# Kernel optimization log

Measured on AMD Instinct MI355X. Metric: run time of the kernel, lower is better.

The kernel has to match this reference:

```python
import jax, jax.numpy as jnp
import numpy as np

GRID_SIZE = 5
IMG_H, IMG_W = 256, 192
N_CTRL = GRID_SIZE * GRID_SIZE
RBF_SCALE = 10.0
OFFSET_SCALE = 0.3


def _source_pts():
    # control points on a [-0.9, 0.9] lattice, (N, 2) as (x, y)
    s = jnp.linspace(-0.9, 0.9, GRID_SIZE)
    gy, gx = jnp.meshgrid(s, s, indexing='ij')
    return jnp.stack([gx.ravel(), gy.ravel()], axis=-1)


def _tps_grid(theta):
    B = theta.shape[0]
    src = _source_pts()                                   # (N, 2)
    offsets = theta.reshape(B, N_CTRL, 2) * OFFSET_SCALE  # dx,dy per control pt
    gy = jnp.linspace(-1.0, 1.0, IMG_H)
    gx = jnp.linspace(-1.0, 1.0, IMG_W)
    my, mx = jnp.meshgrid(gy, gx, indexing='ij')          # (H, W)
    # RBF basis per control point: (N, H, W)
    dist = (mx[None] - src[:, 0, None, None]) ** 2 + (my[None] - src[:, 1, None, None]) ** 2
    w = jnp.exp(-dist * RBF_SCALE)
    # accumulate all control-point displacements in one contraction (fused loop)
    ox = jnp.einsum('bn,nhw->bhw', offsets[..., 0], w)
    oy = jnp.einsum('bn,nhw->bhw', offsets[..., 1], w)
    grid = jnp.stack([mx[None] + ox, my[None] + oy], axis=-1)  # (B, H, W, 2)
    return jnp.clip(grid, -1.0, 1.0)


def _grid_sample_border(img, grid):
    # bilinear grid_sample, align_corners=True, padding_mode='border'
    B, C, H, W = img.shape
    x = (grid[..., 0] + 1.0) * 0.5 * (W - 1)
    y = (grid[..., 1] + 1.0) * 0.5 * (H - 1)
    x0f = jnp.floor(x)
    y0f = jnp.floor(y)
    wx = x - x0f
    wy = y - y0f
    x0 = jnp.clip(x0f.astype(jnp.int32), 0, W - 1)
    x1 = jnp.clip(x0f.astype(jnp.int32) + 1, 0, W - 1)
    y0 = jnp.clip(y0f.astype(jnp.int32), 0, H - 1)
    y1 = jnp.clip(y0f.astype(jnp.int32) + 1, 0, H - 1)
    imgc = jnp.transpose(img, (0, 2, 3, 1))               # (B, H, W, C)
    b = jnp.arange(B)[:, None, None]
    Ia = imgc[b, y0, x0]
    Ib = imgc[b, y0, x1]
    Ic = imgc[b, y1, x0]
    Id = imgc[b, y1, x1]
    wa = ((1 - wx) * (1 - wy))[..., None]
    wb = (wx * (1 - wy))[..., None]
    wc = ((1 - wx) * wy)[..., None]
    wd = (wx * wy)[..., None]
    out = wa * Ia + wb * Ib + wc * Ic + wd * Id           # (B, H, W, C)
    return jnp.transpose(out, (0, 3, 1, 2))


def setup_inputs() -> dict:
    key = jax.random.key(0)
    k1, k2 = jax.random.split(key)
    cloth = jax.random.normal(k1, (64, 3, IMG_H, IMG_W), dtype=jnp.float32)
    theta = jax.random.normal(k2, (64, N_CTRL * 2), dtype=jnp.float32)
    return {"cloth": cloth, "theta": theta}


def reference(cloth, theta):
    grid = _tps_grid(theta)
    return _grid_sample_border(cloth, grid)
```

## Files before the change

kernel.cpp:

```cpp
#include <hip/hip_runtime.h>

constexpr int GRID_SZ = 5;
constexpr int N_CTRL  = 25;
constexpr int IMG_H   = 256;
constexpr int IMG_W   = 192;
constexpr int BATCH   = 64;
constexpr int BCHUNK  = 2;
constexpr int PLANE   = IMG_H * IMG_W;
constexpr int PIX_BLOCKS = PLANE / 256;
constexpr int NWG = PIX_BLOCKS * (BATCH / BCHUNK);
constexpr float RBF_SCALE = 10.0f;
constexpr float OFF_SCALE = 0.3f;

typedef float vf2 __attribute__((ext_vector_type(2)));

__device__ __forceinline__ float bilin(float wx, float wy, vf2 r0, vf2 r1) {
    const float top = fmaf(wx, r0[1] - r0[0], r0[0]);
    const float bot = fmaf(wx, r1[1] - r1[0], r1[0]);
    return fmaf(wy, bot - top, top);
}

#define LOAD6(PBASE, VA0, VA1, VB0, VB1, VC0, VC1) do {                        \
    const float* p0_ = (PBASE);                                                \
    const float* p1_ = p0_ + PLANE;                                            \
    const float* p2_ = p1_ + PLANE;                                            \
    asm volatile("global_load_dwordx2 %0, %1, off"            : "=v"(VA0) : "v"(p0_)); \
    asm volatile("global_load_dwordx2 %0, %1, off offset:768" : "=v"(VA1) : "v"(p0_)); \
    asm volatile("global_load_dwordx2 %0, %1, off"            : "=v"(VB0) : "v"(p1_)); \
    asm volatile("global_load_dwordx2 %0, %1, off offset:768" : "=v"(VB1) : "v"(p1_)); \
    asm volatile("global_load_dwordx2 %0, %1, off"            : "=v"(VC0) : "v"(p2_)); \
    asm volatile("global_load_dwordx2 %0, %1, off offset:768" : "=v"(VC1) : "v"(p2_)); \
} while (0)

#define WAIT6(N, V0, V1, V2, V3, V4, V5)                                       \
    asm volatile("s_waitcnt vmcnt(" #N ")"                                     \
                 : "+v"(V0), "+v"(V1), "+v"(V2), "+v"(V3), "+v"(V4), "+v"(V5))

__global__ __launch_bounds__(256, 4) void tps_warp_kernel(
    const float* __restrict__ cloth,
    const float* __restrict__ theta,
    float* __restrict__ out)
{
    const int flat = blockIdx.x;
    const int xcd  = flat & 7;
    const int w    = flat >> 3;
    const int pb   = w % PIX_BLOCKS;
    const int ph   = w / PIX_BLOCKS;
    const int b0   = (xcd * 4 + ph) * BCHUNK;

    const int pix = pb * 256 + threadIdx.x;
    const int hh = pix / IMG_W;
    const int ww = pix - hh * IMG_W;
    const float mx = -1.0f + (2.0f / (IMG_W - 1)) * (float)ww;
    const float my = -1.0f + (2.0f / (IMG_H - 1)) * (float)hh;

#define RB(d) __expf(-(d) * (d) * RBF_SCALE)
    const float ex0 = RB(mx + 0.90f), ex1 = RB(mx + 0.45f), ex2 = RB(mx),
                ex3 = RB(mx - 0.45f), ex4 = RB(mx - 0.90f);
    const float ey0 = RB(my + 0.90f), ey1 = RB(my + 0.45f), ey2 = RB(my),
                ey3 = RB(my - 0.45f), ey4 = RB(my - 0.90f);
#undef RB

    const float* t0 = theta + (size_t)(b0 + 0) * (2 * N_CTRL);
    const float* t1 = theta + (size_t)(b0 + 1) * (2 * N_CTRL);
    float ox0 = 0, oy0 = 0, ox1 = 0, oy1 = 0;
#define TERM(n, EX, EY) {                                                      \
    const float w_ = OFF_SCALE * (EX) * (EY);                                  \
    ox0 = fmaf(t0[2*(n)], w_, ox0); oy0 = fmaf(t0[2*(n)+1], w_, oy0);          \
    ox1 = fmaf(t1[2*(n)], w_, ox1); oy1 = fmaf(t1[2*(n)+1], w_, oy1); }
    TERM( 0, ex0, ey0) TERM( 1, ex1, ey0) TERM( 2, ex2, ey0) TERM( 3, ex3, ey0) TERM( 4, ex4, ey0)
    TERM( 5, ex0, ey1) TERM( 6, ex1, ey1) TERM( 7, ex2, ey1) TERM( 8, ex3, ey1) TERM( 9, ex4, ey1)
    TERM(10, ex0, ey2) TERM(11, ex1, ey2) TERM(12, ex2, ey2) TERM(13, ex3, ey2) TERM(14, ex4, ey2)
    TERM(15, ex0, ey3) TERM(16, ex1, ey3) TERM(17, ex2, ey3) TERM(18, ex3, ey3) TERM(19, ex4, ey3)
    TERM(20, ex0, ey4) TERM(21, ex1, ey4) TERM(22, ex2, ey4) TERM(23, ex3, ey4) TERM(24, ex4, ey4)
#undef TERM

#define COORD(OX, OY, SX, SY)                                                  \
    const float SX = (fminf(fmaxf(mx + (OX), -1.0f), 1.0f) + 1.0f) * (0.5f * (float)(IMG_W - 1)); \
    const float SY = (fminf(fmaxf(my + (OY), -1.0f), 1.0f) + 1.0f) * (0.5f * (float)(IMG_H - 1));
    COORD(ox0, oy0, sx0, sy0)
    COORD(ox1, oy1, sx1, sy1)
#undef COORD

    const size_t img_stride = (size_t)3 * PLANE;
    const float* imgb = cloth + (size_t)b0 * img_stride;
    float*       outb = out   + (size_t)b0 * img_stride + pix;

#define PBASE(B, SX, SY) (imgb + (size_t)(B) * img_stride +                    \
    (size_t)(min((int)(SY), IMG_H - 2) * IMG_W + min((int)(SX), IMG_W - 2)))

    vf2 a0, a1, a2, a3, a4, a5;
    vf2 b0v, b1v, b2v, b3v, b4v, b5v;
    float r00, r01, r02, r10, r11, r12;

#define BLEND(SX, SY, V0, V1, V2, V3, V4, V5, R0, R1, R2) {                    \
    const float wx_ = (SX) - (float)min((int)(SX), IMG_W - 2);                 \
    const float wy_ = (SY) - (float)min((int)(SY), IMG_H - 2);                 \
    R0 = bilin(wx_, wy_, V0, V1);                                              \
    R1 = bilin(wx_, wy_, V2, V3);                                              \
    R2 = bilin(wx_, wy_, V4, V5); }

    LOAD6(PBASE(0, sx0, sy0), a0, a1, a2, a3, a4, a5);
    LOAD6(PBASE(1, sx1, sy1), b0v, b1v, b2v, b3v, b4v, b5v);
    WAIT6(6, a0, a1, a2, a3, a4, a5);
    BLEND(sx0, sy0, a0, a1, a2, a3, a4, a5, r00, r01, r02);
    WAIT6(0, b0v, b1v, b2v, b3v, b4v, b5v);
    BLEND(sx1, sy1, b0v, b1v, b2v, b3v, b4v, b5v, r10, r11, r12);
#undef BLEND
#undef PBASE

    float* o0 = outb;
    float* o1 = outb + img_stride;
    __builtin_nontemporal_store(r00, o0);
    __builtin_nontemporal_store(r01, o0 + PLANE);
    __builtin_nontemporal_store(r02, o0 + 2 * PLANE);
    __builtin_nontemporal_store(r10, o1);
    __builtin_nontemporal_store(r11, o1 + PLANE);
    __builtin_nontemporal_store(r12, o1 + 2 * PLANE);
}

extern "C" void kernel_launch(void* const* d_in, const int* in_sizes, int n_in,
                              void* d_out, int out_size, void* d_ws, size_t ws_size,
                              hipStream_t stream) {
    const float* cloth = (const float*)d_in[0];
    const float* theta = (const float*)d_in[1];
    float* out = (float*)d_out;

    tps_warp_kernel<<<dim3(NWG), dim3(256), 0, stream>>>(cloth, theta, out);
}
```

Baseline: 35.21 us.

## Process two image rows per thread with row-aligned 192-thread blocks

```diff
diff --git a/kernel.cpp b/kernel.cpp
--- a/kernel.cpp
+++ b/kernel.cpp
@@ -1,14 +1,13 @@
 #include <hip/hip_runtime.h>
 
-constexpr int GRID_SZ = 5;
 constexpr int N_CTRL  = 25;
 constexpr int IMG_H   = 256;
 constexpr int IMG_W   = 192;
 constexpr int BATCH   = 64;
-constexpr int BCHUNK  = 2;
+constexpr int BCH     = 2;
 constexpr int PLANE   = IMG_H * IMG_W;
-constexpr int PIX_BLOCKS = PLANE / 256;
-constexpr int NWG = PIX_BLOCKS * (BATCH / BCHUNK);
+constexpr int ROWPAIRS = IMG_H / 2;
+constexpr int NWG = ROWPAIRS * (BATCH / BCH);
 constexpr float RBF_SCALE = 10.0f;
 constexpr float OFF_SCALE = 0.3f;
 
@@ -36,7 +35,7 @@
     asm volatile("s_waitcnt vmcnt(" #N ")"                                     \
                  : "+v"(V0), "+v"(V1), "+v"(V2), "+v"(V3), "+v"(V4), "+v"(V5))
 
-__global__ __launch_bounds__(256, 4) void tps_warp_kernel(
+__global__ __launch_bounds__(192) void tps_warp_kernel(
     const float* __restrict__ cloth,
     const float* __restrict__ theta,
     float* __restrict__ out)
@@ -44,54 +43,65 @@
     const int flat = blockIdx.x;
     const int xcd  = flat & 7;
     const int w    = flat >> 3;
-    const int pb   = w % PIX_BLOCKS;
-    const int ph   = w / PIX_BLOCKS;
-    const int b0   = (xcd * 4 + ph) * BCHUNK;
+    const int rp   = w & (ROWPAIRS - 1);
+    const int ph   = w >> 7;
+    const int b0   = (xcd * 4 + ph) * BCH;
 
-    const int pix = pb * 256 + threadIdx.x;
-    const int hh = pix / IMG_W;
-    const int ww = pix - hh * IMG_W;
-    const float mx = -1.0f + (2.0f / (IMG_W - 1)) * (float)ww;
-    const float my = -1.0f + (2.0f / (IMG_H - 1)) * (float)hh;
+    const int ww = threadIdx.x;
+    const int h0 = 2 * rp;
+    const int h1 = h0 + 1;
+    const float mx  = -1.0f + (2.0f / (IMG_W - 1)) * (float)ww;
+    const float my0 = -1.0f + (2.0f / (IMG_H - 1)) * (float)h0;
+    const float my1 = my0 + (2.0f / (IMG_H - 1));
 
 #define RB(d) __expf(-(d) * (d) * RBF_SCALE)
     const float ex0 = RB(mx + 0.90f), ex1 = RB(mx + 0.45f), ex2 = RB(mx),
                 ex3 = RB(mx - 0.45f), ex4 = RB(mx - 0.90f);
-    const float ey0 = RB(my + 0.90f), ey1 = RB(my + 0.45f), ey2 = RB(my),
-                ey3 = RB(my - 0.45f), ey4 = RB(my - 0.90f);
+    const float ey00 = RB(my0 + 0.90f), ey01 = RB(my0 + 0.45f), ey02 = RB(my0),
+                ey03 = RB(my0 - 0.45f), ey04 = RB(my0 - 0.90f);
+    const float ey10 = RB(my1 + 0.90f), ey11 = RB(my1 + 0.45f), ey12 = RB(my1),
+                ey13 = RB(my1 - 0.45f), ey14 = RB(my1 - 0.90f);
 #undef RB
 
     const float* t0 = theta + (size_t)(b0 + 0) * (2 * N_CTRL);
     const float* t1 = theta + (size_t)(b0 + 1) * (2 * N_CTRL);
-    float ox0 = 0, oy0 = 0, ox1 = 0, oy1 = 0;
-#define TERM(n, EX, EY) {                                                      \
-    const float w_ = OFF_SCALE * (EX) * (EY);                                  \
-    ox0 = fmaf(t0[2*(n)], w_, ox0); oy0 = fmaf(t0[2*(n)+1], w_, oy0);          \
-    ox1 = fmaf(t1[2*(n)], w_, ox1); oy1 = fmaf(t1[2*(n)+1], w_, oy1); }
-    TERM( 0, ex0, ey0) TERM( 1, ex1, ey0) TERM( 2, ex2, ey0) TERM( 3, ex3, ey0) TERM( 4, ex4, ey0)
-    TERM( 5, ex0, ey1) TERM( 6, ex1, ey1) TERM( 7, ex2, ey1) TERM( 8, ex3, ey1) TERM( 9, ex4, ey1)
-    TERM(10, ex0, ey2) TERM(11, ex1, ey2) TERM(12, ex2, ey2) TERM(13, ex3, ey2) TERM(14, ex4, ey2)
-    TERM(15, ex0, ey3) TERM(16, ex1, ey3) TERM(17, ex2, ey3) TERM(18, ex3, ey3) TERM(19, ex4, ey3)
-    TERM(20, ex0, ey4) TERM(21, ex1, ey4) TERM(22, ex2, ey4) TERM(23, ex3, ey4) TERM(24, ex4, ey4)
+    float ox00 = 0, oy00 = 0, ox01 = 0, oy01 = 0;
+    float ox10 = 0, oy10 = 0, ox11 = 0, oy11 = 0;
+#define TERM(n, EX, EY0, EY1) {                                                \
+    const float w0_ = OFF_SCALE * (EX) * (EY0);                                \
+    const float w1_ = OFF_SCALE * (EX) * (EY1);                                \
+    ox00 = fmaf(t0[2*(n)], w0_, ox00); oy00 = fmaf(t0[2*(n)+1], w0_, oy00);    \
+    ox01 = fmaf(t0[2*(n)], w1_, ox01); oy01 = fmaf(t0[2*(n)+1], w1_, oy01);    \
+    ox10 = fmaf(t1[2*(n)], w0_, ox10); oy10 = fmaf(t1[2*(n)+1], w0_, oy10);    \
+    ox11 = fmaf(t1[2*(n)], w1_, ox11); oy11 = fmaf(t1[2*(n)+1], w1_, oy11); }
+    TERM( 0, ex0, ey00, ey10) TERM( 1, ex1, ey00, ey10) TERM( 2, ex2, ey00, ey10) TERM( 3, ex3, ey00, ey10) TERM( 4, ex4, ey00, ey10)
+    TERM( 5, ex0, ey01, ey11) TERM( 6, ex1, ey01, ey11) TERM( 7, ex2, ey01, ey11) TERM( 8, ex3, ey01, ey11) TERM( 9, ex4, ey01, ey11)
+    TERM(10, ex0, ey02, ey12) TERM(11, ex1, ey02, ey12) TERM(12, ex2, ey02, ey12) TERM(13, ex3, ey02, ey12) TERM(14, ex4, ey02, ey12)
+    TERM(15, ex0, ey03, ey13) TERM(16, ex1, ey03, ey13) TERM(17, ex2, ey03, ey13) TERM(18, ex3, ey03, ey13) TERM(19, ex4, ey03, ey13)
+    TERM(20, ex0, ey04, ey14) TERM(21, ex1, ey04, ey14) TERM(22, ex2, ey04, ey14) TERM(23, ex3, ey04, ey14) TERM(24, ex4, ey04, ey14)
 #undef TERM
 
-#define COORD(OX, OY, SX, SY)                                                  \
+#define COORD(OX, OY, MY, SX, SY)                                              \
     const float SX = (fminf(fmaxf(mx + (OX), -1.0f), 1.0f) + 1.0f) * (0.5f * (float)(IMG_W - 1)); \
-    const float SY = (fminf(fmaxf(my + (OY), -1.0f), 1.0f) + 1.0f) * (0.5f * (float)(IMG_H - 1));
-    COORD(ox0, oy0, sx0, sy0)
-    COORD(ox1, oy1, sx1, sy1)
+    const float SY = (fminf(fmaxf((MY) + (OY), -1.0f), 1.0f) + 1.0f) * (0.5f * (float)(IMG_H - 1));
+    COORD(ox00, oy00, my0, sx00, sy00)
+    COORD(ox01, oy01, my1, sx01, sy01)
+    COORD(ox10, oy10, my0, sx10, sy10)
+    COORD(ox11, oy11, my1, sx11, sy11)
 #undef COORD
 
     const size_t img_stride = (size_t)3 * PLANE;
     const float* imgb = cloth + (size_t)b0 * img_stride;
-    float*       outb = out   + (size_t)b0 * img_stride + pix;
 
 #define PBASE(B, SX, SY) (imgb + (size_t)(B) * img_stride +                    \
     (size_t)(min((int)(SY), IMG_H - 2) * IMG_W + min((int)(SX), IMG_W - 2)))
 
     vf2 a0, a1, a2, a3, a4, a5;
     vf2 b0v, b1v, b2v, b3v, b4v, b5v;
-    float r00, r01, r02, r10, r11, r12;
+    vf2 c0, c1, c2, c3, c4, c5;
+    vf2 d0, d1, d2, d3, d4, d5;
+    float r000, r001, r002, r010, r011, r012;
+    float r100, r101, r102, r110, r111, r112;
 
 #define BLEND(SX, SY, V0, V1, V2, V3, V4, V5, R0, R1, R2) {                    \
     const float wx_ = (SX) - (float)min((int)(SX), IMG_W - 2);                 \
@@ -100,23 +110,37 @@
     R1 = bilin(wx_, wy_, V2, V3);                                              \
     R2 = bilin(wx_, wy_, V4, V5); }
 
-    LOAD6(PBASE(0, sx0, sy0), a0, a1, a2, a3, a4, a5);
-    LOAD6(PBASE(1, sx1, sy1), b0v, b1v, b2v, b3v, b4v, b5v);
+    LOAD6(PBASE(0, sx00, sy00), a0, a1, a2, a3, a4, a5);
+    LOAD6(PBASE(0, sx01, sy01), b0v, b1v, b2v, b3v, b4v, b5v);
     WAIT6(6, a0, a1, a2, a3, a4, a5);
-    BLEND(sx0, sy0, a0, a1, a2, a3, a4, a5, r00, r01, r02);
-    WAIT6(0, b0v, b1v, b2v, b3v, b4v, b5v);
-    BLEND(sx1, sy1, b0v, b1v, b2v, b3v, b4v, b5v, r10, r11, r12);
+    BLEND(sx00, sy00, a0, a1, a2, a3, a4, a5, r000, r001, r002);
+    LOAD6(PBASE(1, sx10, sy10), c0, c1, c2, c3, c4, c5);
+    WAIT6(6, b0v, b1v, b2v, b3v, b4v, b5v);
+    BLEND(sx01, sy01, b0v, b1v, b2v, b3v, b4v, b5v, r010, r011, r012);
+    LOAD6(PBASE(1, sx11, sy11), d0, d1, d2, d3, d4, d5);
+    WAIT6(6, c0, c1, c2, c3, c4, c5);
+    BLEND(sx10, sy10, c0, c1, c2, c3, c4, c5, r100, r101, r102);
+    WAIT6(0, d0, d1, d2, d3, d4, d5);
+    BLEND(sx11, sy11, d0, d1, d2, d3, d4, d5, r110, r111, r112);
 #undef BLEND
 #undef PBASE
 
-    float* o0 = outb;
-    float* o1 = outb + img_stride;
-    __builtin_nontemporal_store(r00, o0);
-    __builtin_nontemporal_store(r01, o0 + PLANE);
-    __builtin_nontemporal_store(r02, o0 + 2 * PLANE);
-    __builtin_nontemporal_store(r10, o1);
-    __builtin_nontemporal_store(r11, o1 + PLANE);
-    __builtin_nontemporal_store(r12, o1 + 2 * PLANE);
+    float* o00 = out + (size_t)(b0 + 0) * img_stride + h0 * IMG_W + ww;
+    float* o01 = o00 + IMG_W;
+    float* o10 = out + (size_t)(b0 + 1) * img_stride + h0 * IMG_W + ww;
+    float* o11 = o10 + IMG_W;
+    __builtin_nontemporal_store(r000, o00);
+    __builtin_nontemporal_store(r001, o00 + PLANE);
+    __builtin_nontemporal_store(r002, o00 + 2 * PLANE);
+    __builtin_nontemporal_store(r010, o01);
+    __builtin_nontemporal_store(r011, o01 + PLANE);
+    __builtin_nontemporal_store(r012, o01 + 2 * PLANE);
+    __builtin_nontemporal_store(r100, o10);
+    __builtin_nontemporal_store(r101, o10 + PLANE);
+    __builtin_nontemporal_store(r102, o10 + 2 * PLANE);
+    __builtin_nontemporal_store(r110, o11);
+    __builtin_nontemporal_store(r111, o11 + PLANE);
+    __builtin_nontemporal_store(r112, o11 + 2 * PLANE);
 }
 
 extern "C" void kernel_launch(void* const* d_in, const int* in_sizes, int n_in,
@@ -126,5 +150,5 @@
     const float* theta = (const float*)d_in[1];
     float* out = (float*)d_out;
 
-    tps_warp_kernel<<<dim3(NWG), dim3(256), 0, stream>>>(cloth, theta, out);
+    tps_warp_kernel<<<dim3(NWG), dim3(192), 0, stream>>>(cloth, theta, out);
 }
```

New measurement: 38.02 us. +8.0%, slower.
